# Kernel optimization log

Hardware: AMD Instinct MI355X
Metric: run time of the kernel (lower is better)

Reference implementation:

```python
import jax, jax.numpy as jnp
import numpy as np

D_MODEL = 1024
HEADS = 16
HEAD_DIM = D_MODEL // HEADS
FF = 4 * D_MODEL
EPS = 1e-5


def _layer_norm(x, g, b):
    mu = jnp.mean(x, axis=-1, keepdims=True)
    var = jnp.mean(jnp.square(x - mu), axis=-1, keepdims=True)
    return (x - mu) * jax.lax.rsqrt(var + EPS) * g + b


def setup_inputs() -> dict:
    key = jax.random.key(0)
    ks = jax.random.split(key, 12)
    s = 0.02
    inp = {
        "x": jax.random.normal(ks[0], (2, 2048, D_MODEL), dtype=jnp.float32),
        "Wq": jax.random.normal(ks[1], (D_MODEL, D_MODEL), dtype=jnp.float32) * s,
        "bq": jnp.zeros((D_MODEL,), jnp.float32),
        "Wk": jax.random.normal(ks[2], (D_MODEL, D_MODEL), dtype=jnp.float32) * s,
        "bk": jnp.zeros((D_MODEL,), jnp.float32),
        "Wv": jax.random.normal(ks[3], (D_MODEL, D_MODEL), dtype=jnp.float32) * s,
        "bv": jnp.zeros((D_MODEL,), jnp.float32),
        "Wm": jax.random.normal(ks[4], (D_MODEL, D_MODEL), dtype=jnp.float32) * s,
        "bm": jnp.zeros((D_MODEL,), jnp.float32),
        "W1": jax.random.normal(ks[5], (D_MODEL, FF), dtype=jnp.float32) * s,
        "b1": jnp.zeros((FF,), jnp.float32),
        "W2": jax.random.normal(ks[6], (FF, D_MODEL), dtype=jnp.float32) * s,
        "b2": jnp.zeros((D_MODEL,), jnp.float32),
        "g1": jnp.ones((D_MODEL,), jnp.float32),
        "be1": jnp.zeros((D_MODEL,), jnp.float32),
        "g2": jnp.ones((D_MODEL,), jnp.float32),
        "be2": jnp.zeros((D_MODEL,), jnp.float32),
    }
    return inp


def reference(x, Wq, bq, Wk, bk, Wv, bv, Wm, bm, W1, b1, W2, b2, g1, be1, g2, be2):
    B, L, _ = x.shape
    # self-attention: source = x, no pos, no masks
    q = (x @ Wq + bq).reshape(B, L, HEADS, HEAD_DIM).transpose(0, 2, 1, 3)
    k = (x @ Wk + bk).reshape(B, L, HEADS, HEAD_DIM).transpose(0, 2, 1, 3)
    v = (x @ Wv + bv).reshape(B, L, HEADS, HEAD_DIM).transpose(0, 2, 1, 3)
    scale = 1.0 / np.sqrt(HEAD_DIM).astype(np.float32)
    scores = jnp.einsum("bhld,bhsd->bhls", q, k) * scale  # [B,H,L,L]
    attn = jax.nn.softmax(scores, axis=-1)
    msg = jnp.einsum("bhls,bhsd->bhld", attn, v)
    msg = msg.transpose(0, 2, 1, 3).reshape(B, L, D_MODEL)
    msg = msg @ Wm + bm
    h = _layer_norm(x + msg, g1, be1)
    ffn = jax.nn.relu(h @ W1 + b1) @ W2 + b2
    return _layer_norm(h + ffn, g2, be2)
```

## Files before the change

kernel.cpp:

```cpp
#include <hip/hip_runtime.h>

#define D_MODEL 1024
#define N_TOK   4096
#define HEADS   16
#define FF_DIM  4096
#define SEQ_L   2048

typedef unsigned short u16;
typedef unsigned int   u32;
typedef __bf16 bf16x8 __attribute__((ext_vector_type(8)));
typedef float  f32x4  __attribute__((ext_vector_type(4)));

#define AS1C(p) ((const __attribute__((address_space(1))) void*)(p))
#define AS3(p)  ((__attribute__((address_space(3))) void*)(p))

__device__ __forceinline__ u16 f2bf(float f) {
    union { float f; unsigned u; } c; c.f = f;
    return (u16)((c.u + 0x7fffu + ((c.u >> 16) & 1u)) >> 16);
}
__device__ __forceinline__ float bf2f(u16 b) {
    union { unsigned u; float f; } c; c.u = ((unsigned)b) << 16;
    return c.f;
}
__device__ __forceinline__ u32 cvt_pk_bf16(float lo, float hi) {
    u32 r;
    asm("v_cvt_pk_bf16_f32 %0, %1, %2" : "=v"(r) : "v"(lo), "v"(hi));
    return r;
}

template<int MFR, int RELU, int OUT_BF16>
__global__ __launch_bounds__(256)
void gemm_bt(const u16* __restrict__ A, const u16* __restrict__ Bt,
             const float* __restrict__ bias, void* __restrict__ Cv,
             int M, int N, int K)
{
    constexpr int BM = MFR * 32;
    __shared__ u16 As[BM * 64];
    __shared__ u16 Bs[128 * 64];

    const int tid  = threadIdx.x;
    const int wid  = tid >> 6, lane = tid & 63;
    const int wr   = wid >> 1, wc = wid & 1;
    const int l15  = lane & 15, l16 = lane >> 4;
    const int r0   = blockIdx.y * BM, c0 = blockIdx.x * 128;

    f32x4 acc[MFR][4];
#pragma unroll
    for (int m = 0; m < MFR; ++m)
#pragma unroll
        for (int n = 0; n < 4; ++n) acc[m][n] = (f32x4){0.f, 0.f, 0.f, 0.f};

    for (int k0 = 0; k0 < K; k0 += 64) {
        __syncthreads();
#pragma unroll
        for (int i = 0; i < BM / 32; ++i) {
            const int rb = wid * (BM / 4) + i * 8;
            const int r  = rb + (lane >> 3);
            const int gc = (lane & 7) ^ (r & 7);
            __builtin_amdgcn_global_load_lds(AS1C(A + (size_t)(r0 + r) * K + k0 + gc * 8),
                                             AS3(&As[rb * 64]), 16, 0, 0);
        }
#pragma unroll
        for (int i = 0; i < 4; ++i) {
            const int rb = wid * 32 + i * 8;
            const int r  = rb + (lane >> 3);
            const int gc = (lane & 7) ^ (r & 7);
            __builtin_amdgcn_global_load_lds(AS1C(Bt + (size_t)(c0 + r) * K + k0 + gc * 8),
                                             AS3(&Bs[rb * 64]), 16, 0, 0);
        }
        __syncthreads();
#pragma unroll
        for (int ks = 0; ks < 2; ++ks) {
            bf16x8 af[MFR], bb[4];
#pragma unroll
            for (int m = 0; m < MFR; ++m) {
                const int row = wr * (MFR * 16) + m * 16 + l15;
                const int ch  = (ks * 4 + l16) ^ (row & 7);
                af[m] = *(const bf16x8*)&As[row * 64 + ch * 8];
            }
#pragma unroll
            for (int n = 0; n < 4; ++n) {
                const int row = wc * 64 + n * 16 + l15;
                const int ch  = (ks * 4 + l16) ^ (row & 7);
                bb[n] = *(const bf16x8*)&Bs[row * 64 + ch * 8];
            }
#pragma unroll
            for (int m = 0; m < MFR; ++m)
#pragma unroll
                for (int n = 0; n < 4; ++n)
                    acc[m][n] = __builtin_amdgcn_mfma_f32_16x16x32_bf16(af[m], bb[n], acc[m][n], 0, 0, 0);
        }
    }

#pragma unroll
    for (int n = 0; n < 4; ++n) {
        const int col = c0 + wc * 64 + n * 16 + l15;
        const float bv = bias[col];
#pragma unroll
        for (int m = 0; m < MFR; ++m) {
#pragma unroll
            for (int r = 0; r < 4; ++r) {
                const size_t row = (size_t)(r0 + wr * (MFR * 16) + m * 16 + l16 * 4 + r);
                float v = acc[m][n][r] + bv;
                if (RELU) v = fmaxf(v, 0.f);
                if (OUT_BF16) ((u16*)Cv)[row * N + col] = f2bf(v);
                else          ((float*)Cv)[row * N + col] = v;
            }
        }
    }
}

__global__ __launch_bounds__(256)
void attn_mfma(const u16* __restrict__ qkv, u16* __restrict__ ao)
{
    __shared__ u16 Kl[64 * 64];
    __shared__ u32 Vt[64 * 32];

    const int tid = threadIdx.x;
    const int wid = tid >> 6, lane = tid & 63;
    const int l15 = lane & 15, l16 = lane >> 4;
    const int bh  = blockIdx.y, b = bh >> 4, h = bh & 15;
    const int ho  = h * 64;
    const size_t tb = (size_t)b * SEQ_L;
    const int q0  = blockIdx.x * 64;

    const u16* qg = qkv + (tb + q0) * 3072 + ho;
    const u16* kg = qkv + tb * 3072 + 1024 + ho;
    const u16* vg = qkv + tb * 3072 + 2048 + ho;

    bf16x8 qa[2];
#pragma unroll
    for (int ks = 0; ks < 2; ++ks)
        qa[ks] = *(const bf16x8*)(qg + (size_t)(wid * 16 + l15) * 3072 + ks * 32 + l16 * 8);

    const int rp = lane & 31;
    const int vc = wid * 2 + (lane >> 5);

    f32x4 oacc[4];
#pragma unroll
    for (int f = 0; f < 4; ++f) oacc[f] = (f32x4){0.f, 0.f, 0.f, 0.f};
    float m_c = -1e30f, l_c = 0.f;

    const float SC = 0.18033688f;

    for (int s0 = 0; s0 < SEQ_L; s0 += 64) {
        union { bf16x8 v; u16 u[8]; } ua, ub;
        ua.v = *(const bf16x8*)(vg + (size_t)(s0 + 2 * rp) * 3072 + vc * 8);
        ub.v = *(const bf16x8*)(vg + (size_t)(s0 + 2 * rp + 1) * 3072 + vc * 8);

        __syncthreads();
#pragma unroll
        for (int i = 0; i < 2; ++i) {
            const int rb = wid * 16 + i * 8;
            const int r  = rb + (lane >> 3);
            const int gc = (lane & 7) ^ (r & 7);
            __builtin_amdgcn_global_load_lds(AS1C(kg + (size_t)(s0 + r) * 3072 + gc * 8),
                                             AS3(&Kl[rb * 64]), 16, 0, 0);
        }
#pragma unroll
        for (int e = 0; e < 8; ++e) {
            const int d = vc * 8 + e;
            const int w = rp ^ (((d & 7) << 2) ^ ((d >> 3) << 1));
            Vt[d * 32 + w] = (u32)ua.u[e] | ((u32)ub.u[e] << 16);
        }
        __syncthreads();

        f32x4 sacc[4];
#pragma unroll
        for (int f = 0; f < 4; ++f) sacc[f] = (f32x4){0.f, 0.f, 0.f, 0.f};
#pragma unroll
        for (int ks = 0; ks < 2; ++ks)
#pragma unroll
            for (int f = 0; f < 4; ++f) {
                const int row = f * 16 + l15;
                const int ch  = (ks * 4 + l16) ^ (row & 7);
                bf16x8 kb = *(const bf16x8*)&Kl[row * 64 + ch * 8];
                sacc[f] = __builtin_amdgcn_mfma_f32_16x16x32_bf16(kb, qa[ks], sacc[f], 0, 0, 0);
            }
#pragma unroll
        for (int f = 0; f < 4; ++f) sacc[f] *= SC;

        float mx = sacc[0][0];
#pragma unroll
        for (int f = 0; f < 4; ++f)
#pragma unroll
            for (int r = 0; r < 4; ++r) mx = fmaxf(mx, sacc[f][r]);
        mx = fmaxf(mx, __shfl_xor(mx, 16));
        mx = fmaxf(mx, __shfl_xor(mx, 32));

        if (__any(mx > m_c + 8.f)) {
            const float mnew = fmaxf(m_c, mx);
            const float corr = __builtin_exp2f(m_c - mnew);
            m_c = mnew;
            l_c *= corr;
#pragma unroll
            for (int r = 0; r < 4; ++r) {
                const float cr = __shfl(corr, l16 * 4 + r);
#pragma unroll
                for (int f = 0; f < 4; ++f) oacc[f][r] *= cr;
            }
        }

        float rs = 0.f;
#pragma unroll
        for (int f = 0; f < 4; ++f)
#pragma unroll
            for (int r = 0; r < 4; ++r) {
                const float p = __builtin_exp2f(sacc[f][r] - m_c);
                sacc[f][r] = p; rs += p;
            }
        rs += __shfl_xor(rs, 16);
        rs += __shfl_xor(rs, 32);
        l_c += rs;

        u32 pk[4][2];
#pragma unroll
        for (int f = 0; f < 4; ++f) {
            pk[f][0] = cvt_pk_bf16(sacc[f][0], sacc[f][1]);
            pk[f][1] = cvt_pk_bf16(sacc[f][2], sacc[f][3]);
        }

#pragma unroll
        for (int S = 0; S < 2; ++S) {
            union { bf16x8 v; u32 u[4]; } af;
            af.u[0] = pk[2 * S][0];     af.u[1] = pk[2 * S][1];
            af.u[2] = pk[2 * S + 1][0]; af.u[3] = pk[2 * S + 1][1];
#pragma unroll
            for (int f2 = 0; f2 < 4; ++f2) {
                const int d = f2 * 16 + l15;
                const int swzd = ((d & 7) << 2) ^ ((d >> 3) << 1);
                union { bf16x8 v; uint2 u[2]; } vb;
                vb.u[0] = *(const uint2*)&Vt[d * 32 + ((16 * S + 2 * l16) ^ swzd)];
                vb.u[1] = *(const uint2*)&Vt[d * 32 + ((16 * S + 8 + 2 * l16) ^ swzd)];
                oacc[f2] = __builtin_amdgcn_mfma_f32_16x16x32_bf16(af.v, vb.v, oacc[f2], 0, 0, 0);
            }
        }
    }

#pragma unroll
    for (int r = 0; r < 4; ++r) {
        const float ld  = __shfl(l_c, l16 * 4 + r);
        const float inv = 1.f / ld;
        const size_t row = tb + q0 + wid * 16 + l16 * 4 + r;
#pragma unroll
        for (int f2 = 0; f2 < 4; ++f2)
            ao[row * 1024 + ho + f2 * 16 + l15] = f2bf(oacc[f2][r] * inv);
    }
}

template<int WB>
__global__ __launch_bounds__(256)
void add_ln(const float* __restrict__ x, const u16* __restrict__ y,
            const float* __restrict__ g, const float* __restrict__ be,
            float* __restrict__ outf, u16* __restrict__ outb)
{
    __shared__ float red[4];
    const int t = blockIdx.x, tid = threadIdx.x;
    const int c = tid * 4, lane = tid & 63, wv = tid >> 6;

    float4 a = *(const float4*)(x + (size_t)t * D_MODEL + c);
    ushort4 yb = *(const ushort4*)(y + (size_t)t * D_MODEL + c);
    float s[4] = {a.x + bf2f(yb.x), a.y + bf2f(yb.y), a.z + bf2f(yb.z), a.w + bf2f(yb.w)};

    float ps = s[0] + s[1] + s[2] + s[3];
#pragma unroll
    for (int off = 32; off > 0; off >>= 1) ps += __shfl_down(ps, off);
    if (lane == 0) red[wv] = ps;
    __syncthreads();
    const float mean = (red[0] + red[1] + red[2] + red[3]) * (1.f / D_MODEL);
    __syncthreads();

    float pv = 0.f;
#pragma unroll
    for (int u = 0; u < 4; ++u) { float d = s[u] - mean; pv += d * d; }
#pragma unroll
    for (int off = 32; off > 0; off >>= 1) pv += __shfl_down(pv, off);
    if (lane == 0) red[wv] = pv;
    __syncthreads();
    const float var = (red[0] + red[1] + red[2] + red[3]) * (1.f / D_MODEL);
    const float inv = rsqrtf(var + 1e-5f);

    float4 g4 = *(const float4*)(g + c);
    float4 b4 = *(const float4*)(be + c);
    float o[4];
#pragma unroll
    for (int u = 0; u < 4; ++u) o[u] = (s[u] - mean) * inv;
    float4 of = {o[0] * g4.x + b4.x, o[1] * g4.y + b4.y, o[2] * g4.z + b4.z, o[3] * g4.w + b4.w};
    *(float4*)(outf + (size_t)t * D_MODEL + c) = of;
    if (WB) {
        ushort4 ob = {f2bf(of.x), f2bf(of.y), f2bf(of.z), f2bf(of.w)};
        *(ushort4*)(outb + (size_t)t * D_MODEL + c) = ob;
    }
}

__global__ __launch_bounds__(256)
void prep(const float* __restrict__ Wq, const float* __restrict__ Wk,
          const float* __restrict__ Wv, const float* __restrict__ Wm,
          const float* __restrict__ W1, const float* __restrict__ W2,
          const float* __restrict__ x,
          const float* __restrict__ bq, const float* __restrict__ bk,
          const float* __restrict__ bv,
          u16* __restrict__ wqkv_t, u16* __restrict__ wm_t,
          u16* __restrict__ w1_t, u16* __restrict__ w2_t,
          u16* __restrict__ xb, float* __restrict__ bqkv)
{
    const int blk = blockIdx.x, tid = threadIdx.x;
    if (blk < 3072) {
        __shared__ float T[64][65];
        const float* src; u16* dst; int K, N, tile;
        if (blk < 256)       { src = Wq; dst = wqkv_t;               K = 1024; N = 1024; tile = blk; }
        else if (blk < 512)  { src = Wk; dst = wqkv_t + 1024 * 1024; K = 1024; N = 1024; tile = blk - 256; }
        else if (blk < 768)  { src = Wv; dst = wqkv_t + 2*1024*1024; K = 1024; N = 1024; tile = blk - 512; }
        else if (blk < 1024) { src = Wm; dst = wm_t;                 K = 1024; N = 1024; tile = blk - 768; }
        else if (blk < 2048) { src = W1; dst = w1_t;                 K = 1024; N = 4096; tile = blk - 1024; }
        else                 { src = W2; dst = w2_t;                 K = 4096; N = 1024; tile = blk - 2048; }
        const int ntn = N >> 6;
        const int n0 = (tile % ntn) * 64, k0 = (tile / ntn) * 64;
        const int rr = tid >> 4, cc = (tid & 15) * 4;
#pragma unroll
        for (int u = 0; u < 4; ++u) {
            const float4 v = *(const float4*)(src + (size_t)(k0 + rr + u * 16) * N + n0 + cc);
            T[rr + u * 16][cc + 0] = v.x; T[rr + u * 16][cc + 1] = v.y;
            T[rr + u * 16][cc + 2] = v.z; T[rr + u * 16][cc + 3] = v.w;
        }
        __syncthreads();
#pragma unroll
        for (int u = 0; u < 4; ++u) {
            const int n = rr + u * 16;
            ushort4 o;
            o.x = f2bf(T[cc + 0][n]); o.y = f2bf(T[cc + 1][n]);
            o.z = f2bf(T[cc + 2][n]); o.w = f2bf(T[cc + 3][n]);
            *(ushort4*)(dst + (size_t)(n0 + n) * K + k0 + cc) = o;
        }
    } else if (blk < 3072 + 4096) {
        const int i = (blk - 3072) * 1024 + tid * 4;
        float4 v = *(const float4*)(x + i);
        ushort4 o = {f2bf(v.x), f2bf(v.y), f2bf(v.z), f2bf(v.w)};
        *(ushort4*)(xb + i) = o;
    } else {
#pragma unroll
        for (int u = 0; u < 12; ++u) {
            const int i = u * 256 + tid;
            bqkv[i] = i < 1024 ? bq[i] : (i < 2048 ? bk[i - 1024] : bv[i - 2048]);
        }
    }
}

extern "C" void kernel_launch(void* const* d_in, const int* in_sizes, int n_in,
                              void* d_out, int out_size, void* d_ws, size_t ws_size,
                              hipStream_t stream)
{
    (void)in_sizes; (void)n_in; (void)out_size; (void)ws_size;

    const float* x   = (const float*)d_in[0];
    const float* Wq  = (const float*)d_in[1];
    const float* bq  = (const float*)d_in[2];
    const float* Wk  = (const float*)d_in[3];
    const float* bk  = (const float*)d_in[4];
    const float* Wv  = (const float*)d_in[5];
    const float* bv  = (const float*)d_in[6];
    const float* Wm  = (const float*)d_in[7];
    const float* bm  = (const float*)d_in[8];
    const float* W1  = (const float*)d_in[9];
    const float* b1  = (const float*)d_in[10];
    const float* W2  = (const float*)d_in[11];
    const float* b2  = (const float*)d_in[12];
    const float* g1  = (const float*)d_in[13];
    const float* be1 = (const float*)d_in[14];
    const float* g2  = (const float*)d_in[15];
    const float* be2 = (const float*)d_in[16];
    float* out = (float*)d_out;

    char* base = (char*)d_ws;
    const size_t MB = 1u << 20;
    u16*   wqkv_t = (u16*)(base);
    u16*   wm_t   = (u16*)(base + 6 * MB);
    u16*   w1_t   = (u16*)(base + 8 * MB);
    u16*   w2_t   = (u16*)(base + 16 * MB);
    float* bqkv   = (float*)(base + 24 * MB);
    u16*   xb     = (u16*)(base + 25 * MB);
    u16*   qkv    = (u16*)(base + 33 * MB);
    u16*   ao     = (u16*)(base + 57 * MB);
    u16*   f1     = (u16*)(base + 33 * MB);
    u16*   msg    = (u16*)(base + 25 * MB);
    u16*   ffn    = (u16*)(base + 25 * MB);
    float* hf     = (float*)(base + 65 * MB);
    u16*   hb     = (u16*)(base + 81 * MB);

    dim3 blk(256);
    prep<<<dim3(3072 + 4096 + 1), blk, 0, stream>>>(Wq, Wk, Wv, Wm, W1, W2, x,
                                                    bq, bk, bv,
                                                    wqkv_t, wm_t, w1_t, w2_t, xb, bqkv);

    gemm_bt<4, 0, 1><<<dim3(24, 32), blk, 0, stream>>>(xb, wqkv_t, bqkv, qkv, N_TOK, 3072, 1024);
    attn_mfma<<<dim3(SEQ_L / 64, 32), blk, 0, stream>>>(qkv, ao);
    gemm_bt<2, 0, 1><<<dim3(8, 64), blk, 0, stream>>>(ao, wm_t, bm, msg, N_TOK, 1024, 1024);
    add_ln<1><<<dim3(N_TOK), blk, 0, stream>>>(x, msg, g1, be1, hf, hb);
    gemm_bt<4, 1, 1><<<dim3(32, 32), blk, 0, stream>>>(hb, w1_t, b1, f1, N_TOK, FF_DIM, 1024);
    gemm_bt<2, 0, 1><<<dim3(8, 64), blk, 0, stream>>>(f1, w2_t, b2, ffn, N_TOK, 1024, FF_DIM);
    add_ln<0><<<dim3(N_TOK), blk, 0, stream>>>(hf, ffn, g2, be2, out, nullptr);
}
```

Measured before the change: 283.0 us.

## Add double-buffered 256x256 GEMM and process two query sets per attention block

Adds a 512-thread GEMM kernel with 256x256 tiles and double-buffered LDS. Global-to-LDS loads for the next K slices are interleaved with MFMA phases, using explicit vmcnt waits, barriers and raised wave priority. It is used for the QKV and FFN1 projections. The attention kernel now handles 128 queries per block, so each K fragment loaded from LDS serves two query sets, and the softmax scale is folded into Q at load time. The large tiles leave fewer blocks than CUs for the QKV GEMM, and the roughly 128KB of LDS allows only one block per CU.

Measured after the change: 268.1 us. -5.3%, faster.

```diff
diff --git a/kernel.cpp b/kernel.cpp
--- a/kernel.cpp
+++ b/kernel.cpp
@@ -26,6 +26,126 @@
     u32 r;
     asm("v_cvt_pk_bf16_f32 %0, %1, %2" : "=v"(r) : "v"(lo), "v"(hi));
     return r;
+}
+
+template<int RELU>
+__global__ __launch_bounds__(512, 2)
+void gemm_pipe(const u16* __restrict__ A, const u16* __restrict__ Bt,
+               const float* __restrict__ bias, u16* __restrict__ C,
+               int M, int N, int K)
+{
+    __shared__ u16 As[2][256 * 64];
+    __shared__ u16 Bs[2][256 * 64];
+
+    const int tid = threadIdx.x;
+    const int wid = tid >> 6, lane = tid & 63;
+    const int wr  = wid >> 2, wc = wid & 3;
+    const int l15 = lane & 15, l16 = lane >> 4;
+    const int r0  = blockIdx.y * 256, c0 = blockIdx.x * 256;
+
+    const u16* Ab = A  + (size_t)r0 * K;
+    const u16* Bb = Bt + (size_t)c0 * K;
+
+    f32x4 acc[8][4];
+#pragma unroll
+    for (int m = 0; m < 8; ++m)
+#pragma unroll
+        for (int n = 0; n < 4; ++n) acc[m][n] = (f32x4){0.f, 0.f, 0.f, 0.f};
+
+    auto stage = [&](u16* dst, const u16* src, int kbase) {
+#pragma unroll
+        for (int i = 0; i < 4; ++i) {
+            const int r  = i * 64 + (tid >> 3);
+            const int gc = (tid & 7) ^ (r & 7);
+            __builtin_amdgcn_global_load_lds(AS1C(src + (size_t)r * K + kbase + gc * 8),
+                                             AS3(dst + (i * 64 + (wid << 3)) * 64), 16, 0, 0);
+        }
+    };
+
+    bf16x8 af[4][2], bbA[2][2], bbB[2][2];
+
+    auto ldAf = [&](const u16* sl, int mh) {
+#pragma unroll
+        for (int m = 0; m < 4; ++m) {
+            const int row = wr * 128 + (mh * 4 + m) * 16 + l15;
+#pragma unroll
+            for (int ks = 0; ks < 2; ++ks) {
+                const int ch = (ks * 4 + l16) ^ (row & 7);
+                af[m][ks] = *(const bf16x8*)&sl[row * 64 + ch * 8];
+            }
+        }
+    };
+    auto ldBf = [&](const u16* sl, int pair, bf16x8 (&bb)[2][2]) {
+#pragma unroll
+        for (int n = 0; n < 2; ++n) {
+            const int row = wc * 64 + (pair * 2 + n) * 16 + l15;
+#pragma unroll
+            for (int ks = 0; ks < 2; ++ks) {
+                const int ch = (ks * 4 + l16) ^ (row & 7);
+                bb[n][ks] = *(const bf16x8*)&sl[row * 64 + ch * 8];
+            }
+        }
+    };
+    auto mm16 = [&](int mh, int pair, bf16x8 (&bb)[2][2]) {
+        __builtin_amdgcn_s_setprio(1);
+#pragma unroll
+        for (int ks = 0; ks < 2; ++ks)
+#pragma unroll
+            for (int m = 0; m < 4; ++m)
+#pragma unroll
+                for (int n = 0; n < 2; ++n)
+                    acc[mh * 4 + m][pair * 2 + n] =
+                        __builtin_amdgcn_mfma_f32_16x16x32_bf16(af[m][ks], bb[n][ks],
+                                                                acc[mh * 4 + m][pair * 2 + n], 0, 0, 0);
+        __builtin_amdgcn_s_setprio(0);
+    };
+
+    const int nt = K >> 6;
+    stage(&As[0][0], Ab, 0);
+    stage(&Bs[0][0], Bb, 0);
+    stage(&As[1][0], Ab, 64);
+
+    for (int t = 0; t < nt; ++t) {
+        u16* Asl = &As[t & 1][0];
+        u16* Bsl = &Bs[t & 1][0];
+        u16* Aso = &As[t & 1][0];
+        u16* Bso = &Bs[(t + 1) & 1][0];
+
+        if (t + 1 < nt) { asm volatile("s_waitcnt vmcnt(4)" ::: "memory"); }
+        else            { asm volatile("s_waitcnt vmcnt(0)" ::: "memory"); }
+        __builtin_amdgcn_s_barrier();
+        ldAf(Asl, 0);
+        ldBf(Bsl, 0, bbA);
+        if (t + 1 < nt) stage(Bso, Bb, (t + 1) * 64);
+        __builtin_amdgcn_s_barrier();
+        mm16(0, 0, bbA);
+        __builtin_amdgcn_s_barrier();
+        ldBf(Bsl, 1, bbB);
+        mm16(0, 1, bbB);
+        __builtin_amdgcn_s_barrier();
+        ldAf(Asl, 1);
+        mm16(1, 0, bbA);
+        __builtin_amdgcn_s_barrier();
+        if (t + 2 < nt) stage(Aso, Ab, (t + 2) * 64);
+        mm16(1, 1, bbB);
+        __builtin_amdgcn_s_barrier();
+    }
+
+#pragma unroll
+    for (int n = 0; n < 4; ++n) {
+        const int col = c0 + wc * 64 + n * 16 + l15;
+        const float bv = bias[col];
+#pragma unroll
+        for (int m = 0; m < 8; ++m) {
+#pragma unroll
+            for (int r = 0; r < 4; ++r) {
+                const size_t row = (size_t)(r0 + wr * 128 + m * 16 + l16 * 4 + r);
+                float v = acc[m][n][r] + bv;
+                if (RELU) v = fmaxf(v, 0.f);
+                C[row * N + col] = f2bf(v);
+            }
+        }
+    }
 }
 
 template<int MFR, int RELU, int OUT_BF16>
@@ -122,26 +242,36 @@
     const int bh  = blockIdx.y, b = bh >> 4, h = bh & 15;
     const int ho  = h * 64;
     const size_t tb = (size_t)b * SEQ_L;
-    const int q0  = blockIdx.x * 64;
+    const int q0  = blockIdx.x * 128;
 
     const u16* qg = qkv + (tb + q0) * 3072 + ho;
     const u16* kg = qkv + tb * 3072 + 1024 + ho;
     const u16* vg = qkv + tb * 3072 + 2048 + ho;
 
-    bf16x8 qa[2];
-#pragma unroll
-    for (int ks = 0; ks < 2; ++ks)
-        qa[ks] = *(const bf16x8*)(qg + (size_t)(wid * 16 + l15) * 3072 + ks * 32 + l16 * 8);
+    const float SC = 0.18033688f;
+
+    bf16x8 qa[2][2];
+#pragma unroll
+    for (int set = 0; set < 2; ++set)
+#pragma unroll
+        for (int ks = 0; ks < 2; ++ks) {
+            union { bf16x8 v; u16 u[8]; u32 w[4]; } a, r;
+            a.v = *(const bf16x8*)(qg + (size_t)(wid * 32 + set * 16 + l15) * 3072 + ks * 32 + l16 * 8);
+#pragma unroll
+            for (int e = 0; e < 4; ++e)
+                r.w[e] = cvt_pk_bf16(bf2f(a.u[2 * e]) * SC, bf2f(a.u[2 * e + 1]) * SC);
+            qa[set][ks] = r.v;
+        }
 
     const int rp = lane & 31;
     const int vc = wid * 2 + (lane >> 5);
 
-    f32x4 oacc[4];
-#pragma unroll
-    for (int f = 0; f < 4; ++f) oacc[f] = (f32x4){0.f, 0.f, 0.f, 0.f};
-    float m_c = -1e30f, l_c = 0.f;
-
-    const float SC = 0.18033688f;
+    f32x4 oacc[2][4];
+#pragma unroll
+    for (int set = 0; set < 2; ++set)
+#pragma unroll
+        for (int f = 0; f < 4; ++f) oacc[set][f] = (f32x4){0.f, 0.f, 0.f, 0.f};
+    float m_c[2] = {-1e30f, -1e30f}, l_c[2] = {0.f, 0.f};
 
     for (int s0 = 0; s0 < SEQ_L; s0 += 64) {
         union { bf16x8 v; u16 u[8]; } ua, ub;
@@ -165,87 +295,96 @@
         }
         __syncthreads();
 
-        f32x4 sacc[4];
-#pragma unroll
-        for (int f = 0; f < 4; ++f) sacc[f] = (f32x4){0.f, 0.f, 0.f, 0.f};
-#pragma unroll
-        for (int ks = 0; ks < 2; ++ks)
-#pragma unroll
-            for (int f = 0; f < 4; ++f) {
+        bf16x8 kb[4][2];
+#pragma unroll
+        for (int f = 0; f < 4; ++f)
+#pragma unroll
+            for (int ks = 0; ks < 2; ++ks) {
                 const int row = f * 16 + l15;
                 const int ch  = (ks * 4 + l16) ^ (row & 7);
-                bf16x8 kb = *(const bf16x8*)&Kl[row * 64 + ch * 8];
-                sacc[f] = __builtin_amdgcn_mfma_f32_16x16x32_bf16(kb, qa[ks], sacc[f], 0, 0, 0);
-            }
-#pragma unroll
-        for (int f = 0; f < 4; ++f) sacc[f] *= SC;
-
-        float mx = sacc[0][0];
-#pragma unroll
-        for (int f = 0; f < 4; ++f)
-#pragma unroll
-            for (int r = 0; r < 4; ++r) mx = fmaxf(mx, sacc[f][r]);
-        mx = fmaxf(mx, __shfl_xor(mx, 16));
-        mx = fmaxf(mx, __shfl_xor(mx, 32));
-
-        if (__any(mx > m_c + 8.f)) {
-            const float mnew = fmaxf(m_c, mx);
-            const float corr = __builtin_exp2f(m_c - mnew);
-            m_c = mnew;
-            l_c *= corr;
-#pragma unroll
-            for (int r = 0; r < 4; ++r) {
-                const float cr = __shfl(corr, l16 * 4 + r);
-#pragma unroll
-                for (int f = 0; f < 4; ++f) oacc[f][r] *= cr;
-            }
-        }
-
-        float rs = 0.f;
-#pragma unroll
-        for (int f = 0; f < 4; ++f)
-#pragma unroll
-            for (int r = 0; r < 4; ++r) {
-                const float p = __builtin_exp2f(sacc[f][r] - m_c);
-                sacc[f][r] = p; rs += p;
-            }
-        rs += __shfl_xor(rs, 16);
-        rs += __shfl_xor(rs, 32);
-        l_c += rs;
-
-        u32 pk[4][2];
-#pragma unroll
-        for (int f = 0; f < 4; ++f) {
-            pk[f][0] = cvt_pk_bf16(sacc[f][0], sacc[f][1]);
-            pk[f][1] = cvt_pk_bf16(sacc[f][2], sacc[f][3]);
-        }
-
-#pragma unroll
-        for (int S = 0; S < 2; ++S) {
-            union { bf16x8 v; u32 u[4]; } af;
-            af.u[0] = pk[2 * S][0];     af.u[1] = pk[2 * S][1];
-            af.u[2] = pk[2 * S + 1][0]; af.u[3] = pk[2 * S + 1][1];
-#pragma unroll
-            for (int f2 = 0; f2 < 4; ++f2) {
-                const int d = f2 * 16 + l15;
-                const int swzd = ((d & 7) << 2) ^ ((d >> 3) << 1);
-                union { bf16x8 v; uint2 u[2]; } vb;
-                vb.u[0] = *(const uint2*)&Vt[d * 32 + ((16 * S + 2 * l16) ^ swzd)];
-                vb.u[1] = *(const uint2*)&Vt[d * 32 + ((16 * S + 8 + 2 * l16) ^ swzd)];
-                oacc[f2] = __builtin_amdgcn_mfma_f32_16x16x32_bf16(af.v, vb.v, oacc[f2], 0, 0, 0);
-            }
-        }
-    }
-
-#pragma unroll
-    for (int r = 0; r < 4; ++r) {
-        const float ld  = __shfl(l_c, l16 * 4 + r);
-        const float inv = 1.f / ld;
-        const size_t row = tb + q0 + wid * 16 + l16 * 4 + r;
-#pragma unroll
-        for (int f2 = 0; f2 < 4; ++f2)
-            ao[row * 1024 + ho + f2 * 16 + l15] = f2bf(oacc[f2][r] * inv);
-    }
+                kb[f][ks] = *(const bf16x8*)&Kl[row * 64 + ch * 8];
+            }
+
+#pragma unroll
+        for (int set = 0; set < 2; ++set) {
+            f32x4 sacc[4];
+#pragma unroll
+            for (int f = 0; f < 4; ++f) sacc[f] = (f32x4){0.f, 0.f, 0.f, 0.f};
+#pragma unroll
+            for (int ks = 0; ks < 2; ++ks)
+#pragma unroll
+                for (int f = 0; f < 4; ++f)
+                    sacc[f] = __builtin_amdgcn_mfma_f32_16x16x32_bf16(kb[f][ks], qa[set][ks], sacc[f], 0, 0, 0);
+
+            float mx = sacc[0][0];
+#pragma unroll
+            for (int f = 0; f < 4; ++f)
+#pragma unroll
+                for (int r = 0; r < 4; ++r) mx = fmaxf(mx, sacc[f][r]);
+            mx = fmaxf(mx, __shfl_xor(mx, 16));
+            mx = fmaxf(mx, __shfl_xor(mx, 32));
+
+            if (__any(mx > m_c[set] + 8.f)) {
+                const float mnew = fmaxf(m_c[set], mx);
+                const float corr = __builtin_exp2f(m_c[set] - mnew);
+                m_c[set] = mnew;
+                l_c[set] *= corr;
+#pragma unroll
+                for (int r = 0; r < 4; ++r) {
+                    const float cr = __shfl(corr, l16 * 4 + r);
+#pragma unroll
+                    for (int f = 0; f < 4; ++f) oacc[set][f][r] *= cr;
+                }
+            }
+
+            float rs = 0.f;
+#pragma unroll
+            for (int f = 0; f < 4; ++f)
+#pragma unroll
+                for (int r = 0; r < 4; ++r) {
+                    const float p = __builtin_exp2f(sacc[f][r] - m_c[set]);
+                    sacc[f][r] = p; rs += p;
+                }
+            rs += __shfl_xor(rs, 16);
+            rs += __shfl_xor(rs, 32);
+            l_c[set] += rs;
+
+            u32 pk[4][2];
+#pragma unroll
+            for (int f = 0; f < 4; ++f) {
+                pk[f][0] = cvt_pk_bf16(sacc[f][0], sacc[f][1]);
+                pk[f][1] = cvt_pk_bf16(sacc[f][2], sacc[f][3]);
+            }
+
+#pragma unroll
+            for (int S = 0; S < 2; ++S) {
+                union { bf16x8 v; u32 u[4]; } af;
+                af.u[0] = pk[2 * S][0];     af.u[1] = pk[2 * S][1];
+                af.u[2] = pk[2 * S + 1][0]; af.u[3] = pk[2 * S + 1][1];
+#pragma unroll
+                for (int f2 = 0; f2 < 4; ++f2) {
+                    const int d = f2 * 16 + l15;
+                    const int swzd = ((d & 7) << 2) ^ ((d >> 3) << 1);
+                    union { bf16x8 v; uint2 u[2]; } vb;
+                    vb.u[0] = *(const uint2*)&Vt[d * 32 + ((16 * S + 2 * l16) ^ swzd)];
+                    vb.u[1] = *(const uint2*)&Vt[d * 32 + ((16 * S + 8 + 2 * l16) ^ swzd)];
+                    oacc[set][f2] = __builtin_amdgcn_mfma_f32_16x16x32_bf16(af.v, vb.v, oacc[set][f2], 0, 0, 0);
+                }
+            }
+        }
+    }
+
+#pragma unroll
+    for (int set = 0; set < 2; ++set)
+#pragma unroll
+        for (int r = 0; r < 4; ++r) {
+            const float ld  = __shfl(l_c[set], l16 * 4 + r);
+            const float inv = 1.f / ld;
+            const size_t row = tb + q0 + wid * 32 + set * 16 + l16 * 4 + r;
+#pragma unroll
+            for (int f2 = 0; f2 < 4; ++f2)
+                ao[row * 1024 + ho + f2 * 16 + l15] = f2bf(oacc[set][f2][r] * inv);
+        }
 }
 
 template<int WB>
@@ -392,11 +531,11 @@
                                                     bq, bk, bv,
                                                     wqkv_t, wm_t, w1_t, w2_t, xb, bqkv);
 
-    gemm_bt<4, 0, 1><<<dim3(24, 32), blk, 0, stream>>>(xb, wqkv_t, bqkv, qkv, N_TOK, 3072, 1024);
-    attn_mfma<<<dim3(SEQ_L / 64, 32), blk, 0, stream>>>(qkv, ao);
+    gemm_pipe<0><<<dim3(12, 16), dim3(512), 0, stream>>>(xb, wqkv_t, bqkv, qkv, N_TOK, 3072, 1024);
+    attn_mfma<<<dim3(SEQ_L / 128, 32), blk, 0, stream>>>(qkv, ao);
     gemm_bt<2, 0, 1><<<dim3(8, 64), blk, 0, stream>>>(ao, wm_t, bm, msg, N_TOK, 1024, 1024);
     add_ln<1><<<dim3(N_TOK), blk, 0, stream>>>(x, msg, g1, be1, hf, hb);
-    gemm_bt<4, 1, 1><<<dim3(32, 32), blk, 0, stream>>>(hb, w1_t, b1, f1, N_TOK, FF_DIM, 1024);
+    gemm_pipe<1><<<dim3(16, 16), dim3(512), 0, stream>>>(hb, w1_t, b1, f1, N_TOK, FF_DIM, 1024);
     gemm_bt<2, 0, 1><<<dim3(8, 64), blk, 0, stream>>>(f1, w2_t, b2, ffn, N_TOK, 1024, FF_DIM);
     add_ln<0><<<dim3(N_TOK), blk, 0, stream>>>(hf, ffn, g2, be2, out, nullptr);
 }
```
